# Optimization experiments

Hardware: AMD Instinct MI355X
Metric: run time of the kernel (lower is better)

Reference implementation:

```python
import jax, jax.numpy as jnp
import numpy as np

B, T, I, H = 64, 512, 256, 512


def _gru_cell(x, h, Wih, Whh, bih, bhh):
    # PyTorch GRUCell math.
    gi = x @ Wih.T + bih          # [B, 3H]
    gh = h @ Whh.T + bhh          # [B, 3H]
    i_r, i_z, i_n = jnp.split(gi, 3, axis=1)
    h_r, h_z, h_n = jnp.split(gh, 3, axis=1)
    r = jax.nn.sigmoid(i_r + h_r)
    z = jax.nn.sigmoid(i_z + h_z)
    n = jnp.tanh(i_n + r * h_n)
    return (1.0 - z) * n + z * h


def setup_inputs() -> dict:
    key = jax.random.key(0)
    ks = jax.random.split(key, 20)
    inp = {"x": jax.random.normal(ks[0], (B, T, I), dtype=jnp.float32)}
    def w(k, shape):
        return (jax.random.normal(k, shape, dtype=jnp.float32) * 0.05)
    idx = 1
    for d in ("f", "b"):
        for j, in_sz in enumerate((I, H)):
            inp[f"Wih_{d}{j}"] = w(ks[idx], (3 * H, in_sz)); idx += 1
            inp[f"Whh_{d}{j}"] = w(ks[idx], (3 * H, H)); idx += 1
            inp[f"bih_{d}{j}"] = w(ks[idx], (3 * H,)); idx += 1
            inp[f"bhh_{d}{j}"] = w(ks[idx], (3 * H,)); idx += 1
    return inp


def reference(x, Wih_f0, Whh_f0, bih_f0, bhh_f0, Wih_f1, Whh_f1, bih_f1, bhh_f1,
              Wih_b0, Whh_b0, bih_b0, bhh_b0, Wih_b1, Whh_b1, bih_b1, bhh_b1):
    b = x.shape[0]
    h0 = jnp.zeros((b, H), dtype=x.dtype)

    def step(carry, xt):
        hf0, hf1, hb0, hb1 = carry
        # NOTE: original flips the FEATURE axis of the step slice (torch.flip(input[:,i,:],[1])),
        # i.e. the backward GRU sees feature-reversed input at the same timestep.
        xb = jnp.flip(xt, axis=1)
        hf0 = _gru_cell(xt, hf0, Wih_f0, Whh_f0, bih_f0, bhh_f0)
        hb0 = _gru_cell(xb, hb0, Wih_b0, Whh_b0, bih_b0, bhh_b0)
        hf1 = _gru_cell(hf0, hf1, Wih_f1, Whh_f1, bih_f1, bhh_f1)
        hb1 = _gru_cell(hb0, hb1, Wih_b1, Whh_b1, bih_b1, bhh_b1)
        return (hf0, hf1, hb0, hb1), jnp.concatenate([hf1, hb1], axis=1)

    _, ys = jax.lax.scan(step, (h0, h0, h0, h0), jnp.swapaxes(x, 0, 1))
    out = jnp.swapaxes(ys, 0, 1)  # [B, T, 2H]
    return out, out[:, -1, :]
```

## Files before the change

kernel.cpp:

```cpp
#include <hip/hip_runtime.h>

#define HH 512
#define II 256
#define TT 512
#define BB 64

typedef unsigned short u16;
typedef unsigned int u32;
typedef unsigned long long u64;
typedef __bf16 bf16x8 __attribute__((ext_vector_type(8)));
typedef u16 u16x8 __attribute__((ext_vector_type(8)));
typedef float f32x4 __attribute__((ext_vector_type(4)));
typedef int i32x4 __attribute__((ext_vector_type(4)));

__device__ i32x4 llvm_amdgcn_raw_buffer_load_i32x4(i32x4 srsrc, int voffset,
                                                   int soffset, int aux)
    __asm("llvm.amdgcn.raw.buffer.load.v4i32");

struct GruParams {
  const float* Wih[4];
  const float* Whh[4];
  const float* bih[4];
  const float* bhh[4];
  const u16* xbf;
  u16* hbuf;
  u32* bar;
  float* out;
};

__device__ __forceinline__ u16 f2bf(float f) {
  u32 u = __builtin_bit_cast(u32, f);
  u += 0x7fffu + ((u >> 16) & 1u);
  return (u16)(u >> 16);
}

__device__ __forceinline__ float sigm(float x) {
  return 1.0f / (1.0f + __expf(-x));
}

__device__ __forceinline__ float tanh_s(float x) {
  float t = __expf(-2.0f * fabsf(x));
  float r = (1.0f - t) / (1.0f + t);
  return copysignf(r, x);
}

__global__ void cvt_x(const float* __restrict__ x, u16* __restrict__ xb) {
  const int i = blockIdx.x * blockDim.x + threadIdx.x;
  const float4 v = reinterpret_cast<const float4*>(x)[i];
  ushort4 o;
  o.x = f2bf(v.x); o.y = f2bf(v.y); o.z = f2bf(v.z); o.w = f2bf(v.w);
  reinterpret_cast<ushort4*>(xb)[i] = o;
}

__global__ __launch_bounds__(256, 1) void gru_persist(GruParams p) {
  const int tid  = threadIdx.x;
  const int lane = tid & 63;
  const int wid  = tid >> 6;

  __shared__ float gsm[4][16][33];
  __shared__ u32 role_sm;

  u32 xcd;
  asm volatile("s_getreg_b32 %0, hwreg(HW_REG_XCC_ID)" : "=s"(xcd));
  xcd &= 7u;
  u32* ctr  = p.bar + 256;
  u32* xcds = p.bar + 257;
  if (tid == 0) xcds[blockIdx.x] = xcd;
  __syncthreads();
  if (tid == 0) {
    __hip_atomic_fetch_add(ctr, 1u, __ATOMIC_RELEASE, __HIP_MEMORY_SCOPE_AGENT);
    while (__hip_atomic_load(ctr, __ATOMIC_RELAXED, __HIP_MEMORY_SCOPE_AGENT) < 256u) {}
    (void)__hip_atomic_load(ctr, __ATOMIC_ACQUIRE, __HIP_MEMORY_SCOPE_AGENT);
    u32 rank = 0;
    for (int w = 0; w < 256; ++w) {
      const u32 xw = xcds[w];
      if (xw == xcd && w < (int)blockIdx.x) rank++;
    }
    role_sm = rank;
  }
  __syncthreads();

  const u32 rank = role_sm;
  const int cell = (xcd < 4) ? (rank < 16 ? 0 : 2) : (rank < 16 ? 1 : 3);
  const int mm   = (int)(xcd & 3u);
  const int cc   = (int)(rank & 15u);

  const int KIN  = (cell < 2) ? II : HH;
  const int n16  = lane & 15;
  const int kg   = (lane >> 4) & 3;
  const int koff = kg * 8;
  const int gb   = (wid == 0) ? 0 : (wid == 1) ? HH : 2 * HH;
  const int nbase = gb + cc * 32;

  int nk, inp_end;
  if (wid < 2)       { nk = (KIN + HH) / 32; inp_end = KIN; }
  else if (wid == 2) { nk = KIN / 32;        inp_end = KIN; }
  else               { nk = HH / 32;         inp_end = 0;   }

  float bias0, bias1;
  {
    const int n0 = nbase + n16, n1 = nbase + 16 + n16;
    if (wid < 2)       { bias0 = p.bih[cell][n0] + p.bhh[cell][n0];
                         bias1 = p.bih[cell][n1] + p.bhh[cell][n1]; }
    else if (wid == 2) { bias0 = p.bih[cell][n0]; bias1 = p.bih[cell][n1]; }
    else               { bias0 = p.bhh[cell][n0]; bias1 = p.bhh[cell][n1]; }
  }

  i32x4 hrs;
  hrs[0] = (int)(u32)(uintptr_t)p.hbuf;
  hrs[1] = (int)(u32)(((u64)(uintptr_t)p.hbuf) >> 32);
  hrs[2] = (int)(4 * 2 * BB * HH * 2);
  hrs[3] = 0x00020000;

  bf16x8 wf[32][2];
  {
    const float* Wih = p.Wih[cell];
    const float* Whh = p.Whh[cell];
    #pragma unroll
    for (int ks = 0; ks < 32; ++ks) {
      if (ks < nk) {
        const int kk = ks * 32;
        #pragma unroll
        for (int j = 0; j < 2; ++j) {
          const int r = nbase + 16 * j + n16;
          u16x8 t;
          if (kk < inp_end) {
            const int col = kk + koff;
            if (cell == 1) {
              #pragma unroll
              for (int e = 0; e < 8; ++e)
                t[e] = f2bf(Wih[r * KIN + (KIN - 1 - (col + e))]);
            } else {
              const float4 a = *reinterpret_cast<const float4*>(Wih + r * KIN + col);
              const float4 b = *reinterpret_cast<const float4*>(Wih + r * KIN + col + 4);
              t[0]=f2bf(a.x); t[1]=f2bf(a.y); t[2]=f2bf(a.z); t[3]=f2bf(a.w);
              t[4]=f2bf(b.x); t[5]=f2bf(b.y); t[6]=f2bf(b.z); t[7]=f2bf(b.w);
            }
          } else {
            const int col = kk - inp_end + koff;
            const float4 a = *reinterpret_cast<const float4*>(Whh + r * HH + col);
            const float4 b = *reinterpret_cast<const float4*>(Whh + r * HH + col + 4);
            t[0]=f2bf(a.x); t[1]=f2bf(a.y); t[2]=f2bf(a.z); t[3]=f2bf(a.w);
            t[4]=f2bf(b.x); t[5]=f2bf(b.y); t[6]=f2bf(b.z); t[7]=f2bf(b.w);
          }
          wf[ks][j] = __builtin_bit_cast(bf16x8, t);
        }
        __builtin_amdgcn_sched_barrier(0);
      }
    }
  }

  u32* dctr = p.bar + xcd * 32;
  const int brow = mm * 16 + n16;
  float h0r = 0.0f, h1r = 0.0f;

  for (int s = 0; s <= TT; ++s) {
    const int tc = (cell < 2) ? s : s - 1;
    const bool active = (tc >= 0) && (tc < TT);
    if (active) {
      const int inp_off = (cell >= 2)
        ? (((cell - 2) * 2 + (tc & 1)) * BB + brow) * HH : 0;
      const int own_off = ((cell * 2 + ((tc & 1) ^ 1)) * BB + brow) * HH;
      const u16* xrow = p.xbf + (size_t)(brow * TT + tc) * II;

      f32x4 acc00 = {bias0, bias0, bias0, bias0};
      f32x4 acc01 = {bias1, bias1, bias1, bias1};
      f32x4 acc10 = {0.f, 0.f, 0.f, 0.f};
      f32x4 acc11 = {0.f, 0.f, 0.f, 0.f};

      #pragma unroll
      for (int blk = 0; blk < 4; ++blk) {
        if (blk * 256 < nk * 32) {
          const int kb = blk * 256;
          const bool is_x = (cell < 2) && (kb < inp_end);
          const int hoff = ((kb < inp_end) ? (inp_off + kb)
                                           : (own_off + (kb - inp_end))) + koff;
          #pragma unroll
          for (int u = 0; u < 8; ++u) {
            bf16x8 af;
            if (is_x) {
              af = __builtin_bit_cast(bf16x8,
                  *reinterpret_cast<const uint4*>(xrow + kb + koff + u * 32));
            } else {
              af = __builtin_bit_cast(bf16x8,
                  llvm_amdgcn_raw_buffer_load_i32x4(hrs, 2 * (hoff + u * 32), 0, 1));
            }
            if (u & 1) {
              acc10 = __builtin_amdgcn_mfma_f32_16x16x32_bf16(af, wf[blk*8+u][0], acc10, 0, 0, 0);
              acc11 = __builtin_amdgcn_mfma_f32_16x16x32_bf16(af, wf[blk*8+u][1], acc11, 0, 0, 0);
            } else {
              acc00 = __builtin_amdgcn_mfma_f32_16x16x32_bf16(af, wf[blk*8+u][0], acc00, 0, 0, 0);
              acc01 = __builtin_amdgcn_mfma_f32_16x16x32_bf16(af, wf[blk*8+u][1], acc01, 0, 0, 0);
            }
          }
        }
      }
      #pragma unroll
      for (int i = 0; i < 4; ++i) {
        gsm[wid][kg * 4 + i][n16]      = acc00[i] + acc10[i];
        gsm[wid][kg * 4 + i][16 + n16] = acc01[i] + acc11[i];
      }
    }
    __syncthreads();
    if (active) {
      #pragma unroll
      for (int q = 0; q < 2; ++q) {
        const int e = tid + q * 256;
        const int row = e >> 5, col = e & 31;
        const float rr = sigm(gsm[0][row][col]);
        const float zz = sigm(gsm[1][row][col]);
        const float nn = tanh_s(gsm[2][row][col] + rr * gsm[3][row][col]);
        const float hp = q ? h1r : h0r;
        const float hn = (1.0f - zz) * nn + zz * hp;
        if (q) h1r = hn; else h0r = hn;
        const int gbrow = mm * 16 + row;
        const int hc = cc * 32 + col;
        p.hbuf[(size_t)((cell * 2 + (tc & 1)) * BB + gbrow) * HH + hc] = f2bf(hn);
      }
    }
    if (s < TT) {
      asm volatile("s_waitcnt vmcnt(0)" ::: "memory");
      __syncthreads();
      if (tid == 0)
        (void)__hip_atomic_fetch_add(dctr, 1u, __ATOMIC_RELAXED,
                                     __HIP_MEMORY_SCOPE_AGENT);
    }
    if (active && cell >= 2) {
      #pragma unroll
      for (int q = 0; q < 2; ++q) {
        const int e = tid + q * 256;
        const int row = e >> 5, col = e & 31;
        const int gbrow = mm * 16 + row;
        const int jb = ((cell == 2) ? 0 : HH) + cc * 32 + col;
        const float hv = q ? h1r : h0r;
        __builtin_nontemporal_store(hv,
            p.out + (size_t)(gbrow * TT + tc) * 1024 + jb);
        if (tc == TT - 1)
          p.out[(size_t)BB * TT * 1024 + (size_t)gbrow * 1024 + jb] = hv;
      }
    }
    if (s < TT) {
      if (tid == 0) {
        const u32 tgt = 32u * (u32)(s + 1);
        while (__hip_atomic_load(dctr, __ATOMIC_RELAXED,
                                 __HIP_MEMORY_SCOPE_AGENT) < tgt) {}
      }
      __syncthreads();
    }
  }
}

extern "C" void kernel_launch(void* const* d_in, const int* in_sizes, int n_in,
                              void* d_out, int out_size, void* d_ws, size_t ws_size,
                              hipStream_t stream) {
  (void)in_sizes; (void)n_in; (void)out_size; (void)ws_size;
  GruParams prm;
  prm.Wih[0] = (const float*)d_in[1];  prm.Whh[0] = (const float*)d_in[2];
  prm.bih[0] = (const float*)d_in[3];  prm.bhh[0] = (const float*)d_in[4];
  prm.Wih[2] = (const float*)d_in[5];  prm.Whh[2] = (const float*)d_in[6];
  prm.bih[2] = (const float*)d_in[7];  prm.bhh[2] = (const float*)d_in[8];
  prm.Wih[1] = (const float*)d_in[9];  prm.Whh[1] = (const float*)d_in[10];
  prm.bih[1] = (const float*)d_in[11]; prm.bhh[1] = (const float*)d_in[12];
  prm.Wih[3] = (const float*)d_in[13]; prm.Whh[3] = (const float*)d_in[14];
  prm.bih[3] = (const float*)d_in[15]; prm.bhh[3] = (const float*)d_in[16];

  const size_t XBF_BYTES  = (size_t)BB * TT * II * 2;
  const size_t HBUF_BYTES = (size_t)4 * 2 * BB * HH * 2;
  u16* xbf  = (u16*)d_ws;
  u16* hbuf = (u16*)((char*)d_ws + XBF_BYTES);
  u32* bar  = (u32*)((char*)d_ws + XBF_BYTES + HBUF_BYTES);

  prm.xbf = xbf; prm.hbuf = hbuf; prm.bar = bar; prm.out = (float*)d_out;

  hipMemsetAsync((char*)d_ws + XBF_BYTES, 0, HBUF_BYTES + 4096, stream);

  const float* x = (const float*)d_in[0];
  cvt_x<<<dim3((BB * TT * II / 4) / 256), dim3(256), 0, stream>>>(x, xbf);

  void* args[] = { &prm };
  hipError_t err = hipLaunchCooperativeKernel((void*)gru_persist, dim3(256), dim3(256),
                                              args, 0, stream);
  if (err != hipSuccess) {
    hipLaunchKernelGGL(gru_persist, dim3(256), dim3(256), 0, stream, prm);
  }
}
```

Measured before the change: 2.745 ms.

## Replace per-XCD counter barrier with per-block step flags and 4-deep h ring

Swaps the per-step counter barrier (atomic add plus spin for all 32 blocks) for per-block progress flags. Each block writes its own flag after a step, and consumers poll only the flags they depend on, with the layer-1 cells allowed to run up to several steps behind layer 0. The hidden-state buffer grows from 2 to 4 slots so the producer can run ahead without overwriting data still being read. Layer-1 cells no longer shift by one step in lockstep, which allows more pipelining between layers. The cost is wider polling loads per wave and reliance on sc0 cache semantics for correctness.

```diff
diff --git a/kernel.cpp b/kernel.cpp
--- a/kernel.cpp
+++ b/kernel.cpp
@@ -63,8 +63,8 @@
   u32 xcd;
   asm volatile("s_getreg_b32 %0, hwreg(HW_REG_XCC_ID)" : "=s"(xcd));
   xcd &= 7u;
-  u32* ctr  = p.bar + 256;
-  u32* xcds = p.bar + 257;
+  u32* ctr  = p.bar + 320;
+  u32* xcds = p.bar + 384;
   if (tid == 0) xcds[blockIdx.x] = xcd;
   __syncthreads();
   if (tid == 0) {
@@ -109,7 +109,7 @@
   i32x4 hrs;
   hrs[0] = (int)(u32)(uintptr_t)p.hbuf;
   hrs[1] = (int)(u32)(((u64)(uintptr_t)p.hbuf) >> 32);
-  hrs[2] = (int)(4 * 2 * BB * HH * 2);
+  hrs[2] = (int)(4 * 4 * BB * HH * 2);
   hrs[3] = 0x00020000;
 
   bf16x8 wf[32][2];
@@ -150,82 +150,106 @@
     }
   }
 
-  u32* dctr = p.bar + xcd * 32;
+  u32* flF = p.bar + xcd * 32;
+  u32* flM = p.bar + 768 + xcd * 32;
   const int brow = mm * 16 + n16;
   float h0r = 0.0f, h1r = 0.0f;
 
-  for (int s = 0; s <= TT; ++s) {
-    const int tc = (cell < 2) ? s : s - 1;
-    const bool active = (tc >= 0) && (tc < TT);
-    if (active) {
-      const int inp_off = (cell >= 2)
-        ? (((cell - 2) * 2 + (tc & 1)) * BB + brow) * HH : 0;
-      const int own_off = ((cell * 2 + ((tc & 1) ^ 1)) * BB + brow) * HH;
-      const u16* xrow = p.xbf + (size_t)(brow * TT + tc) * II;
-
-      f32x4 acc00 = {bias0, bias0, bias0, bias0};
-      f32x4 acc01 = {bias1, bias1, bias1, bias1};
-      f32x4 acc10 = {0.f, 0.f, 0.f, 0.f};
-      f32x4 acc11 = {0.f, 0.f, 0.f, 0.f};
-
-      #pragma unroll
-      for (int blk = 0; blk < 4; ++blk) {
-        if (blk * 256 < nk * 32) {
-          const int kb = blk * 256;
-          const bool is_x = (cell < 2) && (kb < inp_end);
-          const int hoff = ((kb < inp_end) ? (inp_off + kb)
-                                           : (own_off + (kb - inp_end))) + koff;
-          #pragma unroll
-          for (int u = 0; u < 8; ++u) {
-            bf16x8 af;
-            if (is_x) {
-              af = __builtin_bit_cast(bf16x8,
-                  *reinterpret_cast<const uint4*>(xrow + kb + koff + u * 32));
-            } else {
-              af = __builtin_bit_cast(bf16x8,
-                  llvm_amdgcn_raw_buffer_load_i32x4(hrs, 2 * (hoff + u * 32), 0, 1));
-            }
-            if (u & 1) {
-              acc10 = __builtin_amdgcn_mfma_f32_16x16x32_bf16(af, wf[blk*8+u][0], acc10, 0, 0, 0);
-              acc11 = __builtin_amdgcn_mfma_f32_16x16x32_bf16(af, wf[blk*8+u][1], acc11, 0, 0, 0);
-            } else {
-              acc00 = __builtin_amdgcn_mfma_f32_16x16x32_bf16(af, wf[blk*8+u][0], acc00, 0, 0, 0);
-              acc01 = __builtin_amdgcn_mfma_f32_16x16x32_bf16(af, wf[blk*8+u][1], acc01, 0, 0, 0);
-            }
+  for (int tc = 0; tc < TT; ++tc) {
+    {
+      const int l31 = lane & 31;
+      const int thr = (cell < 2) ? ((l31 < 16) ? tc : tc - 3)
+                                 : ((l31 < 16) ? tc + 1 : tc);
+      const u64 fa = (u64)(uintptr_t)(flF + l31);
+      int it = 0;
+      while (true) {
+        u32 v;
+        asm volatile("global_load_dword %0, %1, off sc0\n\t"
+                     "s_waitcnt vmcnt(0)"
+                     : "=v"(v) : "v"(fa) : "memory");
+        const bool ok = (lane >= 32) || ((int)v >= thr);
+        if (__all((int)ok)) break;
+        if (++it >= 8) {
+          it = 0;
+          const u32 w = __hip_atomic_load(flM + l31, __ATOMIC_RELAXED,
+                                          __HIP_MEMORY_SCOPE_AGENT);
+          const bool okm = (lane >= 32) || ((int)w >= thr);
+          if (__all((int)okm)) break;
+        }
+      }
+    }
+
+    const int inp_off = (cell >= 2)
+      ? (((cell - 2) * 4 + (tc & 3)) * BB + brow) * HH : 0;
+    const int own_off = ((cell * 4 + ((tc - 1) & 3)) * BB + brow) * HH;
+    const u16* xrow = p.xbf + (size_t)(brow * TT + tc) * II;
+
+    f32x4 acc00 = {bias0, bias0, bias0, bias0};
+    f32x4 acc01 = {bias1, bias1, bias1, bias1};
+    f32x4 acc10 = {0.f, 0.f, 0.f, 0.f};
+    f32x4 acc11 = {0.f, 0.f, 0.f, 0.f};
+
+    #pragma unroll
+    for (int blk = 0; blk < 4; ++blk) {
+      if (blk * 256 < nk * 32) {
+        const int kb = blk * 256;
+        const bool is_x = (cell < 2) && (kb < inp_end);
+        const int hoff = ((kb < inp_end) ? (inp_off + kb)
+                                         : (own_off + (kb - inp_end))) + koff;
+        #pragma unroll
+        for (int u = 0; u < 8; ++u) {
+          bf16x8 af;
+          if (is_x) {
+            af = __builtin_bit_cast(bf16x8,
+                *reinterpret_cast<const uint4*>(xrow + kb + koff + u * 32));
+          } else {
+            af = __builtin_bit_cast(bf16x8,
+                llvm_amdgcn_raw_buffer_load_i32x4(hrs, 2 * (hoff + u * 32), 0, 1));
+          }
+          if (u & 1) {
+            acc10 = __builtin_amdgcn_mfma_f32_16x16x32_bf16(af, wf[blk*8+u][0], acc10, 0, 0, 0);
+            acc11 = __builtin_amdgcn_mfma_f32_16x16x32_bf16(af, wf[blk*8+u][1], acc11, 0, 0, 0);
+          } else {
+            acc00 = __builtin_amdgcn_mfma_f32_16x16x32_bf16(af, wf[blk*8+u][0], acc00, 0, 0, 0);
+            acc01 = __builtin_amdgcn_mfma_f32_16x16x32_bf16(af, wf[blk*8+u][1], acc01, 0, 0, 0);
           }
         }
       }
-      #pragma unroll
-      for (int i = 0; i < 4; ++i) {
-        gsm[wid][kg * 4 + i][n16]      = acc00[i] + acc10[i];
-        gsm[wid][kg * 4 + i][16 + n16] = acc01[i] + acc11[i];
-      }
+    }
+    #pragma unroll
+    for (int i = 0; i < 4; ++i) {
+      gsm[wid][kg * 4 + i][n16]      = acc00[i] + acc10[i];
+      gsm[wid][kg * 4 + i][16 + n16] = acc01[i] + acc11[i];
     }
     __syncthreads();
-    if (active) {
-      #pragma unroll
-      for (int q = 0; q < 2; ++q) {
-        const int e = tid + q * 256;
-        const int row = e >> 5, col = e & 31;
-        const float rr = sigm(gsm[0][row][col]);
-        const float zz = sigm(gsm[1][row][col]);
-        const float nn = tanh_s(gsm[2][row][col] + rr * gsm[3][row][col]);
-        const float hp = q ? h1r : h0r;
-        const float hn = (1.0f - zz) * nn + zz * hp;
-        if (q) h1r = hn; else h0r = hn;
-        const int gbrow = mm * 16 + row;
-        const int hc = cc * 32 + col;
-        p.hbuf[(size_t)((cell * 2 + (tc & 1)) * BB + gbrow) * HH + hc] = f2bf(hn);
-      }
-    }
-    if (s < TT) {
-      asm volatile("s_waitcnt vmcnt(0)" ::: "memory");
-      __syncthreads();
-      if (tid == 0)
-        (void)__hip_atomic_fetch_add(dctr, 1u, __ATOMIC_RELAXED,
-                                     __HIP_MEMORY_SCOPE_AGENT);
-    }
-    if (active && cell >= 2) {
+
+    #pragma unroll
+    for (int q = 0; q < 2; ++q) {
+      const int e = tid + q * 256;
+      const int row = e >> 5, col = e & 31;
+      const float rr = sigm(gsm[0][row][col]);
+      const float zz = sigm(gsm[1][row][col]);
+      const float nn = tanh_s(gsm[2][row][col] + rr * gsm[3][row][col]);
+      const float hp = q ? h1r : h0r;
+      const float hn = (1.0f - zz) * nn + zz * hp;
+      if (q) h1r = hn; else h0r = hn;
+      const int gbrow = mm * 16 + row;
+      const int hc = cc * 32 + col;
+      p.hbuf[(size_t)((cell * 4 + (tc & 3)) * BB + gbrow) * HH + hc] = f2bf(hn);
+    }
+    asm volatile("s_waitcnt vmcnt(0)" ::: "memory");
+    __syncthreads();
+    if (tid == 0) {
+      const u32 nv = (u32)(tc + 1);
+      __hip_atomic_store(flM + rank, nv, __ATOMIC_RELAXED,
+                         __HIP_MEMORY_SCOPE_AGENT);
+      const u64 fa0 = (u64)(uintptr_t)(flF + rank);
+      asm volatile("global_store_dword %0, %1, off sc0"
+                   :: "v"(fa0), "v"(nv) : "memory");
+    }
+    __syncthreads();
+
+    if (cell >= 2) {
       #pragma unroll
       for (int q = 0; q < 2; ++q) {
         const int e = tid + q * 256;
@@ -238,14 +262,6 @@
         if (tc == TT - 1)
           p.out[(size_t)BB * TT * 1024 + (size_t)gbrow * 1024 + jb] = hv;
       }
-    }
-    if (s < TT) {
-      if (tid == 0) {
-        const u32 tgt = 32u * (u32)(s + 1);
-        while (__hip_atomic_load(dctr, __ATOMIC_RELAXED,
-                                 __HIP_MEMORY_SCOPE_AGENT) < tgt) {}
-      }
-      __syncthreads();
     }
   }
 }
@@ -265,7 +281,7 @@
   prm.bih[3] = (const float*)d_in[15]; prm.bhh[3] = (const float*)d_in[16];
 
   const size_t XBF_BYTES  = (size_t)BB * TT * II * 2;
-  const size_t HBUF_BYTES = (size_t)4 * 2 * BB * HH * 2;
+  const size_t HBUF_BYTES = (size_t)4 * 4 * BB * HH * 2;
   u16* xbf  = (u16*)d_ws;
   u16* hbuf = (u16*)((char*)d_ws + XBF_BYTES);
   u32* bar  = (u32*)((char*)d_ws + XBF_BYTES + HBUF_BYTES);
```

New measurement: 2.689 ms. -2.1%, faster.
